# Kernel tuning notes

Measured on AMD Instinct MI355X. Metric: run time of the kernel, lower is better.

Reference implementation:

```python
import jax, jax.numpy as jnp
import numpy as np

NEG_SLOPE = 0.2  # PyG GATConv leaky_relu slope


def _gat_conv(x, src, dst, W, a_s, a_d, b, H, D, concat):
    """PyG-style GATConv (eval mode, self-loops already in src/dst).
    x: [N, F_in], W: [F_in, H*D], a_s/a_d: [H, D], b: [H*D] or [D]."""
    N = x.shape[0]
    h = (x @ W).reshape(N, H, D)                      # [N, H, D]
    al_src = (h * a_s).sum(-1)                        # [N, H]
    al_dst = (h * a_d).sum(-1)                        # [N, H]
    e = jax.nn.leaky_relu(al_src[src] + al_dst[dst], NEG_SLOPE)   # [E, H]
    m = jax.ops.segment_max(e, dst, num_segments=N)               # [N, H]
    m = jnp.where(jnp.isfinite(m), m, 0.0)
    ex = jnp.exp(e - m[dst])
    denom = jax.ops.segment_sum(ex, dst, num_segments=N)
    alpha = ex / (denom[dst] + 1e-16)                 # edge softmax per dst node
    out = jax.ops.segment_sum(alpha[:, :, None] * h[src], dst, num_segments=N)  # [N, H, D]
    out = out.reshape(N, H * D) if concat else out.mean(axis=1)
    return out + b


def setup_inputs() -> dict:
    key = jax.random.key(0)
    ks = jax.random.split(key, 14)
    N, E, F_in, H, D, OUT = 50000, 800000, 256, 8, 32, 64
    g = lambda k, shape, fan: (jax.random.normal(k, shape, jnp.float32) / np.float32(np.sqrt(fan)))
    return {
        "x": jax.random.normal(ks[0], (N, F_in), jnp.float32),
        "edge_index": jax.random.randint(ks[1], (2, E), 0, N),
        # conv0: GATConv(256 -> 32, heads=8, concat)
        "W0": g(ks[2], (F_in, H * D), F_in),
        "a_src0": g(ks[3], (H, D), D),
        "a_dst0": g(ks[4], (H, D), D),
        "b0": jnp.zeros((H * D,), jnp.float32),
        # residual0: Linear(256 -> 256)
        "Wr0": g(ks[5], (F_in, H * D), F_in),
        "br0": jnp.zeros((H * D,), jnp.float32),
        # conv1: GATConv(256 -> 64, heads=1, concat=False)
        "W1": g(ks[6], (H * D, OUT), H * D),
        "a_src1": g(ks[7], (1, OUT), OUT),
        "a_dst1": g(ks[8], (1, OUT), OUT),
        "b1": jnp.zeros((OUT,), jnp.float32),
        # residual1: Linear(256 -> 64)
        "Wr1": g(ks[9], (H * D, OUT), H * D),
        "br1": jnp.zeros((OUT,), jnp.float32),
    }


def reference(x, edge_index, W0, a_src0, a_dst0, b0, Wr0, br0, W1, a_src1, a_dst1, b1, Wr1, br1):
    N = x.shape[0]
    loops = jnp.arange(N, dtype=edge_index.dtype)
    src = jnp.concatenate([edge_index[0], loops])   # add self loops
    dst = jnp.concatenate([edge_index[1], loops])
    # layer 0: GATConv + residual + ELU (dropout is identity in eval)
    h = _gat_conv(x, src, dst, W0, a_src0, a_dst0, b0, 8, 32, True)
    h = jax.nn.elu(h + (x @ Wr0 + br0))
    # final layer: heads=1, concat=False, + residual
    out = _gat_conv(h, src, dst, W1, a_src1, a_dst1, b1, 1, 64, False)
    out = out + (h @ Wr1 + br1)
    return jax.nn.log_softmax(out, axis=1)
```

## Files before the change

kernel.cpp:

```cpp
#include <hip/hip_runtime.h>
#include <math.h>

#define NEG_SLOPE 0.2f
#define BSH 7
#define NBLK_PART 256

typedef __attribute__((ext_vector_type(8))) short bf16x8;
typedef __attribute__((ext_vector_type(4))) float f32x4;
typedef __attribute__((ext_vector_type(2))) float f32x2;
typedef __attribute__((ext_vector_type(8))) unsigned short ushort8;
typedef __attribute__((ext_vector_type(4))) unsigned short ushort4v;

__device__ __forceinline__ float b2f(unsigned short u){
  return __uint_as_float(((unsigned)u) << 16);
}
__device__ __forceinline__ unsigned short f2b(float f){
  unsigned u = __float_as_uint(f);
  return (unsigned short)((u + 0x7FFFu + ((u >> 16) & 1u)) >> 16);
}

#if __has_builtin(__builtin_amdgcn_cvt_pk_f32_fp8) && __has_builtin(__builtin_amdgcn_cvt_pk_fp8_f32)
#define HW_FP8 1
#else
#define HW_FP8 0
#endif

#if !HW_FP8
__device__ __forceinline__ unsigned enc8_one(float f){
  unsigned bits = __float_as_uint(f);
  unsigned s = bits >> 31;
  unsigned e = (bits >> 23) & 255;
  unsigned mant = bits & 0x7FFFFF;
  if(e < 121){
    float af = fabsf(f);
    int m = (int)(af * 512.f + 0.5f);
    if(m > 7) m = 7;
    return (s << 7) | (unsigned)m;
  }
  unsigned lsb = (mant >> 20) & 1;
  mant += 0x7FFFF + lsb;
  if(mant >> 23){ e += 1; mant = 0; }
  unsigned m3 = mant >> 20;
  unsigned e8 = e - 120;
  if(e8 > 15 || (e8 == 15 && m3 == 7)) return (s << 7) | 0x7E;
  return (s << 7) | (e8 << 3) | m3;
}
#endif

template<bool HI>
__device__ __forceinline__ unsigned enc8_pair(float a, float b, unsigned old){
#if HW_FP8
  return __builtin_amdgcn_cvt_pk_fp8_f32(a, b, old, HI);
#else
  unsigned p = enc8_one(a) | (enc8_one(b) << 8);
  return HI ? ((old & 0x0000FFFFu) | (p << 16)) : ((old & 0xFFFF0000u) | p);
#endif
}

__device__ __forceinline__ void dec8x4v(unsigned q, f32x2& lo, f32x2& hi){
#if HW_FP8
  lo = __builtin_amdgcn_cvt_pk_f32_fp8(q, false);
  hi = __builtin_amdgcn_cvt_pk_f32_fp8(q, true);
#else
  auto dec1 = [](unsigned b)->float{
    unsigned s = (b >> 7) & 1, e = (b >> 3) & 15, m = b & 7;
    float v = (e == 0) ? (float)m * 0.001953125f
                       : __uint_as_float(((e + 120) << 23) | (m << 20));
    return s ? -v : v;
  };
  lo[0] = dec1(q & 255); lo[1] = dec1((q >> 8) & 255);
  hi[0] = dec1((q >> 16) & 255); hi[1] = dec1(q >> 24);
#endif
}

extern "C" __global__ void k_part1(const int* __restrict__ dsts, int E, int N,
                                   int NBUCK, int* __restrict__ bcnt,
                                   int* __restrict__ blockbase){
  __shared__ int hist[512];
  int blk = blockIdx.x, tid = threadIdx.x;
  for(int b = tid; b < NBUCK; b += 256) hist[b] = 0;
  __syncthreads();
  int ET = E + N;
  int chunk = (ET + NBLK_PART - 1)/NBLK_PART;
  int s0 = blk*chunk, s1 = s0+chunk < ET ? s0+chunk : ET;
  for(int e = s0+tid; e < s1; e += 256){
    int d = (e < E) ? dsts[e] : e - E;
    atomicAdd(&hist[d >> BSH], 1);
  }
  __syncthreads();
  for(int b = tid; b < NBUCK; b += 256)
    blockbase[(size_t)blk*NBUCK + b] = atomicAdd(&bcnt[b], hist[b]);
}

extern "C" __global__ void k_bscan(const int* __restrict__ bcnt, int* __restrict__ boffs,
                                   int* __restrict__ offs_last, int NBUCK, int ET){
  __shared__ int sc[512], orig[512];
  int t = threadIdx.x;
  int v = (t < NBUCK) ? bcnt[t] : 0;
  sc[t] = v; orig[t] = v;
  __syncthreads();
  for(int st=1; st<512; st<<=1){
    int u = (t >= st) ? sc[t-st] : 0;
    __syncthreads();
    sc[t] += u;
    __syncthreads();
  }
  if(t < NBUCK) boffs[t] = sc[t] - orig[t];
  if(t == 0){ boffs[NBUCK] = ET; *offs_last = ET; }
}

extern "C" __global__ void k_part2(const int* __restrict__ srcs, const int* __restrict__ dsts,
                                   int E, int N, int NBUCK,
                                   const int* __restrict__ boffs, const int* __restrict__ blockbase,
                                   uint2* __restrict__ pairs){
  __shared__ int cur[512];
  int blk = blockIdx.x, tid = threadIdx.x;
  for(int b = tid; b < NBUCK; b += 256)
    cur[b] = boffs[b] + blockbase[(size_t)blk*NBUCK + b];
  __syncthreads();
  int ET = E + N;
  int chunk = (ET + NBLK_PART - 1)/NBLK_PART;
  int s0 = blk*chunk, s1 = s0+chunk < ET ? s0+chunk : ET;
  for(int e = s0+tid; e < s1; e += 256){
    int s, d;
    if(e < E){ s = srcs[e]; d = dsts[e]; } else { s = d = e - E; }
    int pos = atomicAdd(&cur[d >> BSH], 1);
    uint2 pr; pr.x = (unsigned)d; pr.y = (unsigned)s;
    pairs[pos] = pr;
  }
}

extern "C" __global__ void k_bcsr(const uint2* __restrict__ pairs, const int* __restrict__ boffs,
                                  int N, int* __restrict__ offs, int* __restrict__ csr){
  __shared__ int hist[128], sc[128], lcur[128];
  int b = blockIdx.x, tid = threadIdx.x;
  int node0 = b << BSH;
  int base = boffs[b], endp = boffs[b+1];
  if(tid < 128) hist[tid] = 0;
  __syncthreads();
  for(int i = base + tid; i < endp; i += 256)
    atomicAdd(&hist[pairs[i].x & 127], 1);
  __syncthreads();
  if(tid < 128) sc[tid] = hist[tid];
  __syncthreads();
  for(int st=1; st<128; st<<=1){
    int u = (tid < 128 && tid >= st) ? sc[tid-st] : 0;
    __syncthreads();
    if(tid < 128) sc[tid] += u;
    __syncthreads();
  }
  if(tid < 128){
    int ex = sc[tid] - hist[tid];
    lcur[tid] = ex;
    int n = node0 + tid;
    if(n < N) offs[n] = base + ex;
  }
  __syncthreads();
  for(int i = base + tid; i < endp; i += 256){
    uint2 pr = pairs[i];
    int pos = atomicAdd(&lcur[pr.x & 127], 1);
    csr[base + pos] = (int)pr.y;
  }
}

extern "C" __global__ void k_wt2(const float* __restrict__ W0, const float* __restrict__ Wr0,
                                 const float* __restrict__ W1, const float* __restrict__ Wr1,
                                 unsigned short* __restrict__ WT0, unsigned short* __restrict__ WT1){
  int idx = blockIdx.x*256 + threadIdx.x;
  const int tot0 = 512*256;
  if(idx < tot0){
    int n = idx >> 8, k = idx & 255;
    const float* W = (n < 256) ? W0 : Wr0;
    int c = (n < 256) ? n : n - 256;
    WT0[idx] = f2b(W[(size_t)k*256 + c]);
  } else {
    idx -= tot0;
    if(idx >= 128*256) return;
    int n = idx >> 8, k = idx & 255;
    const float* W = (n < 64) ? W1 : Wr1;
    int c = (n < 64) ? n : n - 64;
    WT1[idx] = f2b(W[(size_t)k*64 + c]);
  }
}

__launch_bounds__(256)
extern "C" __global__ void k_mgemm(const unsigned short* __restrict__ Ab,
                                   const float* __restrict__ Afp,
                                   const unsigned short* __restrict__ WT,
                                   unsigned short* __restrict__ C, int M,
                                   int MB, int NCB, int mode,
                                   unsigned char* __restrict__ qout,
                                   unsigned short* __restrict__ rout,
                                   const float* __restrict__ asv, const float* __restrict__ adv,
                                   float* __restrict__ alsout, float* __restrict__ aldout){
  int id = blockIdx.x;
  int row_blk, col_blk;
  if(NCB == 4){
    col_blk = (id >> 3) & 3;
    row_blk = (id >> 5)*8 + (id & 7);
  } else {
    row_blk = id; col_blk = 0;
  }
  if(row_blk >= MB) return;

  __shared__ unsigned short SH[128*128];
  unsigned short* As = SH;
  unsigned short* Bs = SH + 128*64;
  int t = threadIdx.x;
  int lane = t & 63, wid = t >> 6;
  int wr = wid >> 1, wc = wid & 1;
  int row0 = row_blk*128, col0 = col_blk*128;
  f32x4 acc[4][4] = {};

  float4 v0s[4], v1s[4];
  const float* abase[4];
  if(Afp){
    #pragma unroll
    for(int i=0; i<4; i++){
      int t2 = i*256 + t;
      int r = t2 >> 3;
      int dslot = (t2 & 7) ^ (r & 7);
      int gr = row0 + r; if(gr >= M) gr = M - 1;
      abase[i] = Afp + (size_t)gr*256 + dslot*8;
      v0s[i] = *(const float4*)(abase[i]);
      v1s[i] = *(const float4*)(abase[i] + 4);
    }
  }

  for(int k0 = 0; k0 < 256; k0 += 64){
    if(Afp){
      #pragma unroll
      for(int i=0; i<4; i++){
        ushort8 o;
        o[0]=f2b(v0s[i].x); o[1]=f2b(v0s[i].y); o[2]=f2b(v0s[i].z); o[3]=f2b(v0s[i].w);
        o[4]=f2b(v1s[i].x); o[5]=f2b(v1s[i].y); o[6]=f2b(v1s[i].z); o[7]=f2b(v1s[i].w);
        *(ushort8*)(As + i*2048 + wid*512 + lane*8) = o;
      }
    } else {
      #pragma unroll
      for(int i=0; i<4; i++){
        int t2 = i*256 + t;
        int r = t2 >> 3;
        int dslot = (t2 & 7) ^ (r & 7);
        int gr = row0 + r; if(gr >= M) gr = M - 1;
        const unsigned short* ga = Ab + (size_t)gr*256 + k0 + dslot*8;
        __builtin_amdgcn_global_load_lds((const __attribute__((address_space(1))) unsigned*)ga,
            (__attribute__((address_space(3))) unsigned*)(As + i*2048 + wid*512), 16, 0, 0);
      }
    }
    #pragma unroll
    for(int i=0; i<4; i++){
      int t2 = i*256 + t;
      int r = t2 >> 3;
      int dslot = (t2 & 7) ^ (r & 7);
      const unsigned short* gb = WT + (size_t)(col0 + r)*256 + k0 + dslot*8;
      __builtin_amdgcn_global_load_lds((const __attribute__((address_space(1))) unsigned*)gb,
          (__attribute__((address_space(3))) unsigned*)(Bs + i*2048 + wid*512), 16, 0, 0);
    }
    __syncthreads();
    if(Afp && k0 < 192){
      #pragma unroll
      for(int i=0; i<4; i++){
        v0s[i] = *(const float4*)(abase[i] + k0 + 64);
        v1s[i] = *(const float4*)(abase[i] + k0 + 68);
      }
    }
    #pragma unroll
    for(int kc=0; kc<2; kc++){
      bf16x8 a[4], b[4];
      int kb = kc*4 + (lane >> 4);
      #pragma unroll
      for(int f=0; f<4; f++){
        int ar = wr*64 + f*16 + (lane & 15);
        a[f] = *(const bf16x8*)&As[ar*64 + ((kb ^ (ar & 7))*8)];
        int br = wc*64 + f*16 + (lane & 15);
        b[f] = *(const bf16x8*)&Bs[br*64 + ((kb ^ (br & 7))*8)];
      }
      #pragma unroll
      for(int fm=0; fm<4; fm++)
        #pragma unroll
        for(int fn=0; fn<4; fn++)
          acc[fm][fn] = __builtin_amdgcn_mfma_f32_16x16x32_bf16(a[fm], b[fn], acc[fm][fn], 0, 0, 0);
    }
    __syncthreads();
  }

  unsigned short* CT = SH;
  int cg = t & 15;
  #pragma unroll
  for(int half=0; half<2; half++){
    __syncthreads();
    if(wr == half){
      #pragma unroll
      for(int fm=0; fm<4; fm++){
        int rbase = fm*16 + ((lane>>4)<<2);
        #pragma unroll
        for(int r=0; r<4; r++)
          #pragma unroll
          for(int fn=0; fn<4; fn++)
            CT[(rbase+r)*136 + wc*64 + (lane&15) + fn*16] = f2b(acc[fm][fn][r]);
      }
    }
    __syncthreads();
    if(mode == 0){
      bool attn = col_blk < 2;
      int colbase = col0 + cg*8;
      float4 as_lo, as_hi, ad_lo, ad_hi;
      if(attn){
        as_lo = *(const float4*)(asv + colbase);
        as_hi = *(const float4*)(asv + colbase + 4);
        ad_lo = *(const float4*)(adv + colbase);
        ad_hi = *(const float4*)(adv + colbase + 4);
      }
      #pragma unroll
      for(int it=0; it<4; it++){
        int rl = it*16 + (t>>4);
        int row = row0 + half*64 + rl;
        ushort8 vr = *(ushort8*)&CT[rl*136 + cg*8];
        if(attn){
          float f0=b2f(vr[0]),f1=b2f(vr[1]),f2=b2f(vr[2]),f3=b2f(vr[3]);
          float f4=b2f(vr[4]),f5=b2f(vr[5]),f6=b2f(vr[6]),f7=b2f(vr[7]);
          float sd = f0*as_lo.x+f1*as_lo.y+f2*as_lo.z+f3*as_lo.w
                   + f4*as_hi.x+f5*as_hi.y+f6*as_hi.z+f7*as_hi.w;
          float dd = f0*ad_lo.x+f1*ad_lo.y+f2*ad_lo.z+f3*ad_lo.w
                   + f4*ad_hi.x+f5*ad_hi.y+f6*ad_hi.z+f7*ad_hi.w;
          sd += __shfl_xor(sd,1); sd += __shfl_xor(sd,2);
          dd += __shfl_xor(dd,1); dd += __shfl_xor(dd,2);
          uint2 q;
          q.x = enc8_pair<false>(f0,f1,0u); q.x = enc8_pair<true>(f2,f3,q.x);
          q.y = enc8_pair<false>(f4,f5,0u); q.y = enc8_pair<true>(f6,f7,q.y);
          if(row < M){
            *(uint2*)(qout + (size_t)row*256 + colbase) = q;
            if((t&3)==0){
              int head = colbase >> 5;
              alsout[row*8 + head] = sd;
              aldout[row*8 + head] = dd;
            }
          }
        } else {
          if(row < M)
            *(ushort8*)(rout + (size_t)row*256 + (colbase - 256)) = vr;
        }
      }
    } else {
      #pragma unroll
      for(int it=0; it<4; it++){
        int rl = it*16 + (t>>4);
        int row = row0 + half*64 + rl;
        ushort8 vr = *(ushort8*)&CT[rl*136 + cg*8];
        if(row < M){
          *(ushort8*)(C + (size_t)row*128 + cg*8) = vr;
          if(cg < 8){
            float f0=b2f(vr[0]),f1=b2f(vr[1]),f2=b2f(vr[2]),f3=b2f(vr[3]);
            float f4=b2f(vr[4]),f5=b2f(vr[5]),f6=b2f(vr[6]),f7=b2f(vr[7]);
            uint2 q;
            q.x = enc8_pair<false>(f0,f1,0u); q.x = enc8_pair<true>(f2,f3,q.x);
            q.y = enc8_pair<false>(f4,f5,0u); q.y = enc8_pair<true>(f6,f7,q.y);
            *(uint2*)(qout + (size_t)row*64 + cg*8) = q;
            float sd = f0*asv[cg*8+0]+f1*asv[cg*8+1]+f2*asv[cg*8+2]+f3*asv[cg*8+3]
                     + f4*asv[cg*8+4]+f5*asv[cg*8+5]+f6*asv[cg*8+6]+f7*asv[cg*8+7];
            float dd = f0*adv[cg*8+0]+f1*adv[cg*8+1]+f2*adv[cg*8+2]+f3*adv[cg*8+3]
                     + f4*adv[cg*8+4]+f5*adv[cg*8+5]+f6*adv[cg*8+6]+f7*adv[cg*8+7];
            sd += __shfl_xor(sd,1); sd += __shfl_xor(sd,2); sd += __shfl_xor(sd,4);
            dd += __shfl_xor(dd,1); dd += __shfl_xor(dd,2); dd += __shfl_xor(dd,4);
            if((t&15)==0){
              alsout[row] = sd;
              aldout[row] = dd;
            }
          }
        }
      }
    }
  }
}

__launch_bounds__(256)
extern "C" __global__ void k_gather0(const unsigned short* __restrict__ r0b,
                                     const unsigned char* __restrict__ h0q,
                                     const float* __restrict__ als0, const float* __restrict__ ald0,
                                     const int* __restrict__ offs, const int* __restrict__ csr,
                                     const float* __restrict__ b0, const float* __restrict__ br0,
                                     unsigned short* __restrict__ h1b, int N){
  int n = blockIdx.x*4 + (threadIdx.x >> 6);
  if(n >= N) return;
  int lane = threadIdx.x & 63;
  int hh = lane & 7;
  int es = lane >> 3;
  int h  = es;
  int c  = lane*4;
  float ald_h = ald0[n*8 + hh];
  int beg = offs[n], end = offs[n+1];

  f32x2 A01 = {0.f, 0.f}, A23 = {0.f, 0.f};
  float den = 0.f;

  for(int chunk = beg; chunk < end; chunk += 8){
    int m = end - chunk; if(m > 8) m = 8;
    bool e_ok = es < m;
    int s = e_ok ? csr[chunk + es] : 0;
    float p = 0.f;
    if(e_ok){
      float v = als0[s*8 + hh] + ald_h;
      v = v > 0.f ? v : NEG_SLOPE*v;
      p = expf(v);
    }
    den += p;
    int sj[8]; float pj[8];
    #pragma unroll
    for(int j=0; j<8; j++){
      sj[j] = __shfl(s, j*8);
      pj[j] = __shfl(p, j*8 + h);
    }
    unsigned q[8];
    #pragma unroll
    for(int j=0; j<8; j++)
      q[j] = *(const unsigned*)(h0q + (size_t)sj[j]*256 + c);
    #pragma unroll
    for(int j=0; j<8; j++){
      f32x2 lo, hi, pv;
      dec8x4v(q[j], lo, hi);
      pv[0] = pj[j]; pv[1] = pj[j];
      A01 += pv*lo; A23 += pv*hi;
    }
  }

  den += __shfl_xor(den, 8);
  den += __shfl_xor(den, 16);
  den += __shfl_xor(den, 32);
  float rden = 1.f/(den + 1e-16f);
  rden = __shfl(rden, h);

  float a0 = A01[0]*rden, a1 = A01[1]*rden, a2 = A23[0]*rden, a3 = A23[1]*rden;

  float4 bb = *(const float4*)(b0 + c);
  float4 rb = *(const float4*)(br0 + c);
  uint2 ru = *(const uint2*)(r0b + (size_t)n*256 + c);
  float o0 = a0 + bb.x + __uint_as_float(ru.x << 16)         + rb.x;
  float o1 = a1 + bb.y + __uint_as_float(ru.x & 0xFFFF0000u) + rb.y;
  float o2 = a2 + bb.z + __uint_as_float(ru.y << 16)         + rb.z;
  float o3 = a3 + bb.w + __uint_as_float(ru.y & 0xFFFF0000u) + rb.w;
  ushort4v o;
  o[0] = f2b(o0 > 0.f ? o0 : expf(o0) - 1.f);
  o[1] = f2b(o1 > 0.f ? o1 : expf(o1) - 1.f);
  o[2] = f2b(o2 > 0.f ? o2 : expf(o2) - 1.f);
  o[3] = f2b(o3 > 0.f ? o3 : expf(o3) - 1.f);
  *(ushort4v*)(h1b + (size_t)n*256 + c) = o;
}

__launch_bounds__(256)
extern "C" __global__ void k_gather1(const unsigned short* __restrict__ buf1b,
                                     const unsigned char* __restrict__ g1q,
                                     const float* __restrict__ als1, const float* __restrict__ ald1,
                                     const int* __restrict__ offs, const int* __restrict__ csr,
                                     const float* __restrict__ b1, const float* __restrict__ br1,
                                     float* __restrict__ out, int N){
  int n = blockIdx.x*4 + (threadIdx.x >> 6);
  if(n >= N) return;
  int lane = threadIdx.x & 63;
  int ch4 = lane & 15;
  int es  = lane >> 4;
  int c   = ch4*4;
  int beg = offs[n], end = offs[n+1];
  float ald_n = ald1[n];

  f32x2 A01 = {0.f, 0.f}, A23 = {0.f, 0.f};
  float den = 0.f;

  for(int chunk = beg; chunk < end; chunk += 64){
    int m = end - chunk; if(m > 64) m = 64;
    int s = (lane < m) ? csr[chunk + lane] : 0;
    float p = 0.f;
    if(lane < m){
      float v = als1[s] + ald_n;
      v = v > 0.f ? v : NEG_SLOPE*v;
      p = expf(v);
    }
    den += p;
    for(int base = 0; base < m; base += 16){
      int sv[4]; float pv[4];
      #pragma unroll
      for(int i=0; i<4; i++){
        int j = base + 4*i + es;
        int jj = j & 63;
        sv[i] = __shfl(s, jj);
        pv[i] = __shfl(p, jj);
      }
      unsigned qv[4];
      #pragma unroll
      for(int i=0; i<4; i++)
        qv[i] = *(const unsigned*)(g1q + (size_t)sv[i]*64 + c);
      #pragma unroll
      for(int i=0; i<4; i++){
        f32x2 lo, hi, pp;
        dec8x4v(qv[i], lo, hi);
        pp[0] = pv[i]; pp[1] = pv[i];
        A01 += pp*lo; A23 += pp*hi;
      }
    }
  }

  A01[0] += __shfl_xor(A01[0], 16); A01[1] += __shfl_xor(A01[1], 16);
  A23[0] += __shfl_xor(A23[0], 16); A23[1] += __shfl_xor(A23[1], 16);
  A01[0] += __shfl_xor(A01[0], 32); A01[1] += __shfl_xor(A01[1], 32);
  A23[0] += __shfl_xor(A23[0], 32); A23[1] += __shfl_xor(A23[1], 32);
  #pragma unroll
  for(int o=32; o>0; o>>=1) den += __shfl_xor(den, o);
  float rden = 1.f/(den + 1e-16f);

  float4 bb = *(const float4*)(b1 + c);
  float4 rb = *(const float4*)(br1 + c);
  uint2 ru = *(const uint2*)(buf1b + (size_t)n*128 + 64 + c);
  float v0 = A01[0]*rden + bb.x + __uint_as_float(ru.x << 16)         + rb.x;
  float v1 = A01[1]*rden + bb.y + __uint_as_float(ru.x & 0xFFFF0000u) + rb.y;
  float v2 = A23[0]*rden + bb.z + __uint_as_float(ru.y << 16)         + rb.z;
  float v3 = A23[1]*rden + bb.w + __uint_as_float(ru.y & 0xFFFF0000u) + rb.w;

  float mx = fmaxf(fmaxf(v0, v1), fmaxf(v2, v3));
  #pragma unroll
  for(int o=1; o<16; o<<=1) mx = fmaxf(mx, __shfl_xor(mx, o));
  float sm = expf(v0-mx) + expf(v1-mx) + expf(v2-mx) + expf(v3-mx);
  #pragma unroll
  for(int o=1; o<16; o<<=1) sm += __shfl_xor(sm, o);
  float l = mx + logf(sm);
  if(es == 0){
    float4 ov; ov.x = v0-l; ov.y = v1-l; ov.z = v2-l; ov.w = v3-l;
    *(float4*)(out + (size_t)n*64 + c) = ov;
  }
}

extern "C" void kernel_launch(void* const* d_in, const int* in_sizes, int n_in,
                              void* d_out, int out_size, void* d_ws, size_t ws_size,
                              hipStream_t stream){
  const float* x   = (const float*)d_in[0];
  const int*   ei  = (const int*)  d_in[1];
  const float* W0  = (const float*)d_in[2];
  const float* as0 = (const float*)d_in[3];
  const float* ad0 = (const float*)d_in[4];
  const float* b0  = (const float*)d_in[5];
  const float* Wr0 = (const float*)d_in[6];
  const float* br0 = (const float*)d_in[7];
  const float* W1  = (const float*)d_in[8];
  const float* as1 = (const float*)d_in[9];
  const float* ad1 = (const float*)d_in[10];
  const float* b1  = (const float*)d_in[11];
  const float* Wr1 = (const float*)d_in[12];
  const float* br1 = (const float*)d_in[13];
  int N = in_sizes[0] / 256;
  int E = in_sizes[1] / 2;
  const int* srcs = ei;
  const int* dsts = ei + E;
  float* out = (float*)d_out;

  int ET = E + N;
  int NBUCK = (N + 127) >> BSH;

  unsigned short* r0b   = (unsigned short*)d_ws;
  unsigned char*  h0q   = (unsigned char*)(r0b + (size_t)N*256);
  unsigned short* h1b   = (unsigned short*)(h0q + (size_t)N*256);
  unsigned short* buf1b = h1b + (size_t)N*256;
  unsigned short* WT0   = buf1b + (size_t)N*128;
  unsigned short* WT1   = WT0   + 512*256;
  float*    als0 = (float*)(WT1 + 128*256);
  float*    ald0 = als0 + (size_t)N*8;
  float*    als1 = ald0 + (size_t)N*8;
  float*    ald1 = als1 + N;
  int*      offs = (int*)(ald1 + N);
  int*      bcnt = offs + N + 1;
  int*      boffs = bcnt + NBUCK;
  int*      blockbase = boffs + NBUCK + 1;
  int*      csr  = blockbase + (size_t)NBLK_PART*NBUCK;
  uint2*    pairs = (uint2*)(csr + ET);
  pairs = (uint2*)(((uintptr_t)pairs + 7) & ~(uintptr_t)7);
  unsigned char* g1q = (unsigned char*)(pairs + ET);

  hipMemsetAsync(bcnt, 0, (size_t)NBUCK*sizeof(int), stream);
  hipLaunchKernelGGL(k_part1, dim3(NBLK_PART), dim3(256), 0, stream, dsts, E, N, NBUCK, bcnt, blockbase);
  hipLaunchKernelGGL(k_bscan, dim3(1), dim3(512), 0, stream, bcnt, boffs, offs + N, NBUCK, ET);
  hipLaunchKernelGGL(k_part2, dim3(NBLK_PART), dim3(256), 0, stream, srcs, dsts, E, N, NBUCK, boffs, blockbase, pairs);
  hipLaunchKernelGGL(k_bcsr, dim3(NBUCK), dim3(256), 0, stream, pairs, boffs, N, offs, csr);

  hipLaunchKernelGGL(k_wt2, dim3((512*256+128*256+255)/256), dim3(256), 0, stream, W0, Wr0, W1, Wr1, WT0, WT1);

  int MB = (N + 127) / 128;
  int g0 = ((MB + 7) / 8) * 32;
  hipLaunchKernelGGL(k_mgemm, dim3(g0), dim3(256), 0, stream,
                     (const unsigned short*)nullptr, x, WT0,
                     (unsigned short*)nullptr, N, MB, 4, 0,
                     h0q, r0b, as0, ad0, als0, ald0);
  hipLaunchKernelGGL(k_gather0, dim3((N+3)/4), dim3(256), 0, stream, r0b, h0q, als0, ald0, offs, csr, b0, br0, h1b, N);

  hipLaunchKernelGGL(k_mgemm, dim3(MB), dim3(256), 0, stream,
                     h1b, (const float*)nullptr, WT1,
                     buf1b, N, MB, 1, 1,
                     g1q, (unsigned short*)nullptr,
                     as1, ad1, als1, ald1);
  hipLaunchKernelGGL(k_gather1, dim3((N+3)/4), dim3(256), 0, stream, buf1b, g1q, als1, ald1, offs, csr, b1, br1, out, N);
}
```

Measured before the change: 181.0 us.

## Split GEMM into specialized kernels, double-buffer B tiles, pack edge pairs

Splits the general mgemm into two kernels, one per layer, which removes runtime mode and pointer branches. The layer-0 kernel double-buffers the weight tile in LDS so the next k-slice loads while MFMAs run. It also hoists the attention-vector loads out of the epilogue loop. Separately, the partition step packs each (dst low bits, src) edge pair into a single 32-bit word, halving the traffic for the pairs buffer, but this assumes src fits in 25 bits.

New measurement: 183.3 us. No clear change (+1.3%).

```diff
diff --git a/kernel.cpp b/kernel.cpp
--- a/kernel.cpp
+++ b/kernel.cpp
@@ -112,7 +112,7 @@
 extern "C" __global__ void k_part2(const int* __restrict__ srcs, const int* __restrict__ dsts,
                                    int E, int N, int NBUCK,
                                    const int* __restrict__ boffs, const int* __restrict__ blockbase,
-                                   uint2* __restrict__ pairs){
+                                   unsigned* __restrict__ pairs){
   __shared__ int cur[512];
   int blk = blockIdx.x, tid = threadIdx.x;
   for(int b = tid; b < NBUCK; b += 256)
@@ -125,12 +125,11 @@
     int s, d;
     if(e < E){ s = srcs[e]; d = dsts[e]; } else { s = d = e - E; }
     int pos = atomicAdd(&cur[d >> BSH], 1);
-    uint2 pr; pr.x = (unsigned)d; pr.y = (unsigned)s;
-    pairs[pos] = pr;
-  }
-}
-
-extern "C" __global__ void k_bcsr(const uint2* __restrict__ pairs, const int* __restrict__ boffs,
+    pairs[pos] = ((unsigned)s << 7) | ((unsigned)d & 127u);
+  }
+}
+
+extern "C" __global__ void k_bcsr(const unsigned* __restrict__ pairs, const int* __restrict__ boffs,
                                   int N, int* __restrict__ offs, int* __restrict__ csr){
   __shared__ int hist[128], sc[128], lcur[128];
   int b = blockIdx.x, tid = threadIdx.x;
@@ -139,7 +138,7 @@
   if(tid < 128) hist[tid] = 0;
   __syncthreads();
   for(int i = base + tid; i < endp; i += 256)
-    atomicAdd(&hist[pairs[i].x & 127], 1);
+    atomicAdd(&hist[pairs[i] & 127u], 1);
   __syncthreads();
   if(tid < 128) sc[tid] = hist[tid];
   __syncthreads();
@@ -157,9 +156,9 @@
   }
   __syncthreads();
   for(int i = base + tid; i < endp; i += 256){
-    uint2 pr = pairs[i];
-    int pos = atomicAdd(&lcur[pr.x & 127], 1);
-    csr[base + pos] = (int)pr.y;
+    unsigned pr = pairs[i];
+    int pos = atomicAdd(&lcur[pr & 127u], 1);
+    csr[base + pos] = (int)(pr >> 7);
   }
 }
 
@@ -184,28 +183,20 @@
 }
 
 __launch_bounds__(256)
-extern "C" __global__ void k_mgemm(const unsigned short* __restrict__ Ab,
-                                   const float* __restrict__ Afp,
-                                   const unsigned short* __restrict__ WT,
-                                   unsigned short* __restrict__ C, int M,
-                                   int MB, int NCB, int mode,
-                                   unsigned char* __restrict__ qout,
-                                   unsigned short* __restrict__ rout,
-                                   const float* __restrict__ asv, const float* __restrict__ adv,
-                                   float* __restrict__ alsout, float* __restrict__ aldout){
+extern "C" __global__ void k_mgemm0(const float* __restrict__ Afp,
+                                    const unsigned short* __restrict__ WT,
+                                    int M, int MB,
+                                    unsigned char* __restrict__ qout,
+                                    unsigned short* __restrict__ rout,
+                                    const float* __restrict__ asv, const float* __restrict__ adv,
+                                    float* __restrict__ alsout, float* __restrict__ aldout){
   int id = blockIdx.x;
-  int row_blk, col_blk;
-  if(NCB == 4){
-    col_blk = (id >> 3) & 3;
-    row_blk = (id >> 5)*8 + (id & 7);
-  } else {
-    row_blk = id; col_blk = 0;
-  }
+  int col_blk = (id >> 3) & 3;
+  int row_blk = (id >> 5)*8 + (id & 7);
   if(row_blk >= MB) return;
 
-  __shared__ unsigned short SH[128*128];
+  __shared__ unsigned short SH[24576];
   unsigned short* As = SH;
-  unsigned short* Bs = SH + 128*64;
   int t = threadIdx.x;
   int lane = t & 63, wid = t >> 6;
   int wr = wid >> 1, wc = wid & 1;
@@ -214,51 +205,46 @@
 
   float4 v0s[4], v1s[4];
   const float* abase[4];
-  if(Afp){
+  #pragma unroll
+  for(int i=0; i<4; i++){
+    int t2 = i*256 + t;
+    int r = t2 >> 3, dslot = (t2 & 7) ^ (r & 7);
+    int gr = row0 + r; if(gr >= M) gr = M - 1;
+    abase[i] = Afp + (size_t)gr*256 + dslot*8;
+    v0s[i] = *(const float4*)(abase[i]);
+    v1s[i] = *(const float4*)(abase[i] + 4);
+  }
+  #pragma unroll
+  for(int i=0; i<4; i++){
+    int t2 = i*256 + t;
+    int r = t2 >> 3, dslot = (t2 & 7) ^ (r & 7);
+    const unsigned short* gb = WT + (size_t)(col0 + r)*256 + dslot*8;
+    __builtin_amdgcn_global_load_lds((const __attribute__((address_space(1))) unsigned*)gb,
+        (__attribute__((address_space(3))) unsigned*)(SH + 8192 + i*2048 + wid*512), 16, 0, 0);
+  }
+
+  #pragma unroll
+  for(int ks=0; ks<4; ks++){
+    const int k0 = ks*64;
+    unsigned short* Bc = SH + 8192 + (ks & 1)*8192;
+    unsigned short* Bn = SH + 8192 + ((ks & 1) ^ 1)*8192;
     #pragma unroll
     for(int i=0; i<4; i++){
-      int t2 = i*256 + t;
-      int r = t2 >> 3;
-      int dslot = (t2 & 7) ^ (r & 7);
-      int gr = row0 + r; if(gr >= M) gr = M - 1;
-      abase[i] = Afp + (size_t)gr*256 + dslot*8;
-      v0s[i] = *(const float4*)(abase[i]);
-      v1s[i] = *(const float4*)(abase[i] + 4);
-    }
-  }
-
-  for(int k0 = 0; k0 < 256; k0 += 64){
-    if(Afp){
-      #pragma unroll
-      for(int i=0; i<4; i++){
-        ushort8 o;
-        o[0]=f2b(v0s[i].x); o[1]=f2b(v0s[i].y); o[2]=f2b(v0s[i].z); o[3]=f2b(v0s[i].w);
-        o[4]=f2b(v1s[i].x); o[5]=f2b(v1s[i].y); o[6]=f2b(v1s[i].z); o[7]=f2b(v1s[i].w);
-        *(ushort8*)(As + i*2048 + wid*512 + lane*8) = o;
-      }
-    } else {
+      ushort8 o;
+      o[0]=f2b(v0s[i].x); o[1]=f2b(v0s[i].y); o[2]=f2b(v0s[i].z); o[3]=f2b(v0s[i].w);
+      o[4]=f2b(v1s[i].x); o[5]=f2b(v1s[i].y); o[6]=f2b(v1s[i].z); o[7]=f2b(v1s[i].w);
+      *(ushort8*)(As + i*2048 + wid*512 + lane*8) = o;
+    }
+    __syncthreads();
+    if(ks < 3){
       #pragma unroll
       for(int i=0; i<4; i++){
         int t2 = i*256 + t;
-        int r = t2 >> 3;
-        int dslot = (t2 & 7) ^ (r & 7);
-        int gr = row0 + r; if(gr >= M) gr = M - 1;
-        const unsigned short* ga = Ab + (size_t)gr*256 + k0 + dslot*8;
-        __builtin_amdgcn_global_load_lds((const __attribute__((address_space(1))) unsigned*)ga,
-            (__attribute__((address_space(3))) unsigned*)(As + i*2048 + wid*512), 16, 0, 0);
-      }
-    }
-    #pragma unroll
-    for(int i=0; i<4; i++){
-      int t2 = i*256 + t;
-      int r = t2 >> 3;
-      int dslot = (t2 & 7) ^ (r & 7);
-      const unsigned short* gb = WT + (size_t)(col0 + r)*256 + k0 + dslot*8;
-      __builtin_amdgcn_global_load_lds((const __attribute__((address_space(1))) unsigned*)gb,
-          (__attribute__((address_space(3))) unsigned*)(Bs + i*2048 + wid*512), 16, 0, 0);
-    }
-    __syncthreads();
-    if(Afp && k0 < 192){
+        int r = t2 >> 3, dslot = (t2 & 7) ^ (r & 7);
+        const unsigned short* gb = WT + (size_t)(col0 + r)*256 + (k0 + 64) + dslot*8;
+        __builtin_amdgcn_global_load_lds((const __attribute__((address_space(1))) unsigned*)gb,
+            (__attribute__((address_space(3))) unsigned*)(Bn + i*2048 + wid*512), 16, 0, 0);
+      }
       #pragma unroll
       for(int i=0; i<4; i++){
         v0s[i] = *(const float4*)(abase[i] + k0 + 64);
@@ -274,7 +260,7 @@
         int ar = wr*64 + f*16 + (lane & 15);
         a[f] = *(const bf16x8*)&As[ar*64 + ((kb ^ (ar & 7))*8)];
         int br = wc*64 + f*16 + (lane & 15);
-        b[f] = *(const bf16x8*)&Bs[br*64 + ((kb ^ (br & 7))*8)];
+        b[f] = *(const bf16x8*)&Bc[br*64 + ((kb ^ (br & 7))*8)];
       }
       #pragma unroll
       for(int fm=0; fm<4; fm++)
@@ -287,6 +273,15 @@
 
   unsigned short* CT = SH;
   int cg = t & 15;
+  bool attn = col_blk < 2;
+  int colbase = col0 + cg*8;
+  float4 as_lo, as_hi, ad_lo, ad_hi;
+  if(attn){
+    as_lo = *(const float4*)(asv + colbase);
+    as_hi = *(const float4*)(asv + colbase + 4);
+    ad_lo = *(const float4*)(adv + colbase);
+    ad_hi = *(const float4*)(adv + colbase + 4);
+  }
   #pragma unroll
   for(int half=0; half<2; half++){
     __syncthreads();
@@ -302,71 +297,133 @@
       }
     }
     __syncthreads();
-    if(mode == 0){
-      bool attn = col_blk < 2;
-      int colbase = col0 + cg*8;
-      float4 as_lo, as_hi, ad_lo, ad_hi;
+    #pragma unroll
+    for(int it=0; it<4; it++){
+      int rl = it*16 + (t>>4);
+      int row = row0 + half*64 + rl;
+      ushort8 vr = *(ushort8*)&CT[rl*136 + cg*8];
       if(attn){
-        as_lo = *(const float4*)(asv + colbase);
-        as_hi = *(const float4*)(asv + colbase + 4);
-        ad_lo = *(const float4*)(adv + colbase);
-        ad_hi = *(const float4*)(adv + colbase + 4);
-      }
-      #pragma unroll
-      for(int it=0; it<4; it++){
-        int rl = it*16 + (t>>4);
-        int row = row0 + half*64 + rl;
-        ushort8 vr = *(ushort8*)&CT[rl*136 + cg*8];
-        if(attn){
+        float f0=b2f(vr[0]),f1=b2f(vr[1]),f2=b2f(vr[2]),f3=b2f(vr[3]);
+        float f4=b2f(vr[4]),f5=b2f(vr[5]),f6=b2f(vr[6]),f7=b2f(vr[7]);
+        float sd = f0*as_lo.x+f1*as_lo.y+f2*as_lo.z+f3*as_lo.w
+                 + f4*as_hi.x+f5*as_hi.y+f6*as_hi.z+f7*as_hi.w;
+        float dd = f0*ad_lo.x+f1*ad_lo.y+f2*ad_lo.z+f3*ad_lo.w
+                 + f4*ad_hi.x+f5*ad_hi.y+f6*ad_hi.z+f7*ad_hi.w;
+        sd += __shfl_xor(sd,1); sd += __shfl_xor(sd,2);
+        dd += __shfl_xor(dd,1); dd += __shfl_xor(dd,2);
+        uint2 q;
+        q.x = enc8_pair<false>(f0,f1,0u); q.x = enc8_pair<true>(f2,f3,q.x);
+        q.y = enc8_pair<false>(f4,f5,0u); q.y = enc8_pair<true>(f6,f7,q.y);
+        if(row < M){
+          *(uint2*)(qout + (size_t)row*256 + colbase) = q;
+          if((t&3)==0){
+            int head = colbase >> 5;
+            alsout[row*8 + head] = sd;
+            aldout[row*8 + head] = dd;
+          }
+        }
+      } else {
+        if(row < M)
+          *(ushort8*)(rout + (size_t)row*256 + (colbase - 256)) = vr;
+      }
+    }
+  }
+}
+
+__launch_bounds__(256)
+extern "C" __global__ void k_mgemm1(const unsigned short* __restrict__ Ab,
+                                    const unsigned short* __restrict__ WT,
+                                    unsigned short* __restrict__ C, int M, int MB,
+                                    unsigned char* __restrict__ qout,
+                                    const float* __restrict__ asv, const float* __restrict__ adv,
+                                    float* __restrict__ alsout, float* __restrict__ aldout){
+  int row_blk = blockIdx.x;
+  if(row_blk >= MB) return;
+
+  __shared__ unsigned short SH[128*128];
+  unsigned short* As = SH;
+  unsigned short* Bs = SH + 128*64;
+  int t = threadIdx.x;
+  int lane = t & 63, wid = t >> 6;
+  int wr = wid >> 1, wc = wid & 1;
+  int row0 = row_blk*128;
+  f32x4 acc[4][4] = {};
+
+  for(int k0 = 0; k0 < 256; k0 += 64){
+    #pragma unroll
+    for(int i=0; i<4; i++){
+      int t2 = i*256 + t;
+      int r = t2 >> 3;
+      int dslot = (t2 & 7) ^ (r & 7);
+      int gr = row0 + r; if(gr >= M) gr = M - 1;
+      const unsigned short* ga = Ab + (size_t)gr*256 + k0 + dslot*8;
+      __builtin_amdgcn_global_load_lds((const __attribute__((address_space(1))) unsigned*)ga,
+          (__attribute__((address_space(3))) unsigned*)(As + i*2048 + wid*512), 16, 0, 0);
+      const unsigned short* gb = WT + (size_t)r*256 + k0 + dslot*8;
+      __builtin_amdgcn_global_load_lds((const __attribute__((address_space(1))) unsigned*)gb,
+          (__attribute__((address_space(3))) unsigned*)(Bs + i*2048 + wid*512), 16, 0, 0);
+    }
+    __syncthreads();
+    #pragma unroll
+    for(int kc=0; kc<2; kc++){
+      bf16x8 a[4], b[4];
+      int kb = kc*4 + (lane >> 4);
+      #pragma unroll
+      for(int f=0; f<4; f++){
+        int ar = wr*64 + f*16 + (lane & 15);
+        a[f] = *(const bf16x8*)&As[ar*64 + ((kb ^ (ar & 7))*8)];
+        int br = wc*64 + f*16 + (lane & 15);
+        b[f] = *(const bf16x8*)&Bs[br*64 + ((kb ^ (br & 7))*8)];
+      }
+      #pragma unroll
+      for(int fm=0; fm<4; fm++)
+        #pragma unroll
+        for(int fn=0; fn<4; fn++)
+          acc[fm][fn] = __builtin_amdgcn_mfma_f32_16x16x32_bf16(a[fm], b[fn], acc[fm][fn], 0, 0, 0);
+    }
+    __syncthreads();
+  }
+
+  unsigned short* CT = SH;
+  int cg = t & 15;
+  #pragma unroll
+  for(int half=0; half<2; half++){
+    __syncthreads();
+    if(wr == half){
+      #pragma unroll
+      for(int fm=0; fm<4; fm++){
+        int rbase = fm*16 + ((lane>>4)<<2);
+        #pragma unroll
+        for(int r=0; r<4; r++)
+          #pragma unroll
+          for(int fn=0; fn<4; fn++)
+            CT[(rbase+r)*136 + wc*64 + (lane&15) + fn*16] = f2b(acc[fm][fn][r]);
+      }
+    }
+    __syncthreads();
+    #pragma unroll
+    for(int it=0; it<4; it++){
+      int rl = it*16 + (t>>4);
+      int row = row0 + half*64 + rl;
+      ushort8 vr = *(ushort8*)&CT[rl*136 + cg*8];
+      if(row < M){
+        *(ushort8*)(C + (size_t)row*128 + cg*8) = vr;
+        if(cg < 8){
           float f0=b2f(vr[0]),f1=b2f(vr[1]),f2=b2f(vr[2]),f3=b2f(vr[3]);
           float f4=b2f(vr[4]),f5=b2f(vr[5]),f6=b2f(vr[6]),f7=b2f(vr[7]);
-          float sd = f0*as_lo.x+f1*as_lo.y+f2*as_lo.z+f3*as_lo.w
-                   + f4*as_hi.x+f5*as_hi.y+f6*as_hi.z+f7*as_hi.w;
-          float dd = f0*ad_lo.x+f1*ad_lo.y+f2*ad_lo.z+f3*ad_lo.w
-                   + f4*ad_hi.x+f5*ad_hi.y+f6*ad_hi.z+f7*ad_hi.w;
-          sd += __shfl_xor(sd,1); sd += __shfl_xor(sd,2);
-          dd += __shfl_xor(dd,1); dd += __shfl_xor(dd,2);
           uint2 q;
           q.x = enc8_pair<false>(f0,f1,0u); q.x = enc8_pair<true>(f2,f3,q.x);
           q.y = enc8_pair<false>(f4,f5,0u); q.y = enc8_pair<true>(f6,f7,q.y);
-          if(row < M){
-            *(uint2*)(qout + (size_t)row*256 + colbase) = q;
-            if((t&3)==0){
-              int head = colbase >> 5;
-              alsout[row*8 + head] = sd;
-              aldout[row*8 + head] = dd;
-            }
-          }
-        } else {
-          if(row < M)
-            *(ushort8*)(rout + (size_t)row*256 + (colbase - 256)) = vr;
-        }
-      }
-    } else {
-      #pragma unroll
-      for(int it=0; it<4; it++){
-        int rl = it*16 + (t>>4);
-        int row = row0 + half*64 + rl;
-        ushort8 vr = *(ushort8*)&CT[rl*136 + cg*8];
-        if(row < M){
-          *(ushort8*)(C + (size_t)row*128 + cg*8) = vr;
-          if(cg < 8){
-            float f0=b2f(vr[0]),f1=b2f(vr[1]),f2=b2f(vr[2]),f3=b2f(vr[3]);
-            float f4=b2f(vr[4]),f5=b2f(vr[5]),f6=b2f(vr[6]),f7=b2f(vr[7]);
-            uint2 q;
-            q.x = enc8_pair<false>(f0,f1,0u); q.x = enc8_pair<true>(f2,f3,q.x);
-            q.y = enc8_pair<false>(f4,f5,0u); q.y = enc8_pair<true>(f6,f7,q.y);
-            *(uint2*)(qout + (size_t)row*64 + cg*8) = q;
-            float sd = f0*asv[cg*8+0]+f1*asv[cg*8+1]+f2*asv[cg*8+2]+f3*asv[cg*8+3]
-                     + f4*asv[cg*8+4]+f5*asv[cg*8+5]+f6*asv[cg*8+6]+f7*asv[cg*8+7];
-            float dd = f0*adv[cg*8+0]+f1*adv[cg*8+1]+f2*adv[cg*8+2]+f3*adv[cg*8+3]
-                     + f4*adv[cg*8+4]+f5*adv[cg*8+5]+f6*adv[cg*8+6]+f7*adv[cg*8+7];
-            sd += __shfl_xor(sd,1); sd += __shfl_xor(sd,2); sd += __shfl_xor(sd,4);
-            dd += __shfl_xor(dd,1); dd += __shfl_xor(dd,2); dd += __shfl_xor(dd,4);
-            if((t&15)==0){
-              alsout[row] = sd;
-              aldout[row] = dd;
-            }
+          *(uint2*)(qout + (size_t)row*64 + cg*8) = q;
+          float sd = f0*asv[cg*8+0]+f1*asv[cg*8+1]+f2*asv[cg*8+2]+f3*asv[cg*8+3]
+                   + f4*asv[cg*8+4]+f5*asv[cg*8+5]+f6*asv[cg*8+6]+f7*asv[cg*8+7];
+          float dd = f0*adv[cg*8+0]+f1*adv[cg*8+1]+f2*adv[cg*8+2]+f3*adv[cg*8+3]
+                   + f4*adv[cg*8+4]+f5*adv[cg*8+5]+f6*adv[cg*8+6]+f7*adv[cg*8+7];
+          sd += __shfl_xor(sd,1); sd += __shfl_xor(sd,2); sd += __shfl_xor(sd,4);
+          dd += __shfl_xor(dd,1); dd += __shfl_xor(dd,2); dd += __shfl_xor(dd,4);
+          if((t&15)==0){
+            alsout[row] = sd;
+            aldout[row] = dd;
           }
         }
       }
@@ -569,8 +626,7 @@
   int*      boffs = bcnt + NBUCK;
   int*      blockbase = boffs + NBUCK + 1;
   int*      csr  = blockbase + (size_t)NBLK_PART*NBUCK;
-  uint2*    pairs = (uint2*)(csr + ET);
-  pairs = (uint2*)(((uintptr_t)pairs + 7) & ~(uintptr_t)7);
+  unsigned* pairs = (unsigned*)(csr + ET);
   unsigned char* g1q = (unsigned char*)(pairs + ET);
 
   hipMemsetAsync(bcnt, 0, (size_t)NBUCK*sizeof(int), stream);
@@ -583,16 +639,11 @@
 
   int MB = (N + 127) / 128;
   int g0 = ((MB + 7) / 8) * 32;
-  hipLaunchKernelGGL(k_mgemm, dim3(g0), dim3(256), 0, stream,
-                     (const unsigned short*)nullptr, x, WT0,
-                     (unsigned short*)nullptr, N, MB, 4, 0,
-                     h0q, r0b, as0, ad0, als0, ald0);
+  hipLaunchKernelGGL(k_mgemm0, dim3(g0), dim3(256), 0, stream,
+                     x, WT0, N, MB, h0q, r0b, as0, ad0, als0, ald0);
   hipLaunchKernelGGL(k_gather0, dim3((N+3)/4), dim3(256), 0, stream, r0b, h0q, als0, ald0, offs, csr, b0, br0, h1b, N);
 
-  hipLaunchKernelGGL(k_mgemm, dim3(MB), dim3(256), 0, stream,
-                     h1b, (const float*)nullptr, WT1,
-                     buf1b, N, MB, 1, 1,
-                     g1q, (unsigned short*)nullptr,
-                     as1, ad1, als1, ald1);
+  hipLaunchKernelGGL(k_mgemm1, dim3(MB), dim3(256), 0, stream,
+                     h1b, WT1, buf1b, N, MB, g1q, as1, ad1, als1, ald1);
   hipLaunchKernelGGL(k_gather1, dim3((N+3)/4), dim3(256), 0, stream, buf1b, g1q, als1, ald1, offs, csr, b1, br1, out, N);
 }
```
